# Kernel optimization log

Measured on AMD Instinct MI355X. Metric: run time of the kernel, lower is better.

Reference implementation:

```python
import jax, jax.numpy as jnp
import numpy as np

B, T, C = 2, 2048, 1024
H = 16
HD = C // H  # head_size = 64


def setup_inputs() -> dict:
    key = jax.random.key(0)
    k1, k2, k3 = jax.random.split(key, 3)
    x = jax.random.normal(k1, (B, T, C), dtype=jnp.float32)
    W_qkv = jax.random.normal(k2, (C, 3 * C), dtype=jnp.float32) * (1.0 / np.sqrt(C))
    b_qkv = jnp.zeros((3 * C,), dtype=jnp.float32)
    W_proj = jax.random.normal(k3, (C, C), dtype=jnp.float32) * (1.0 / np.sqrt(C))
    b_proj = jnp.zeros((C,), dtype=jnp.float32)
    return {"x": x, "W_qkv": W_qkv, "b_qkv": b_qkv, "W_proj": W_proj, "b_proj": b_proj}


def reference(x, W_qkv, b_qkv, W_proj, b_proj):
    Bc, Tc, Cc = x.shape
    qkv = x @ W_qkv + b_qkv                      # [B,T,3C]
    # Faithful to torch: view(B,T,H,3*HD) then chunk(3,-1) -> per-head interleaved split
    qkv = qkv.reshape(Bc, Tc, H, 3 * HD)
    q = qkv[..., 0 * HD:1 * HD]                  # [B,T,H,HD]
    k = qkv[..., 1 * HD:2 * HD]
    v = qkv[..., 2 * HD:3 * HD]
    # scores: [B,H,T,T]
    att = jnp.einsum('bqhd,bkhd->bhqk', q, k) / np.sqrt(HD)
    causal = jnp.tril(jnp.ones((Tc, Tc), dtype=bool))
    att = jnp.where(causal[None, None, :, :], att, -jnp.inf)
    att = jax.nn.softmax(att, axis=-1)
    out = jnp.einsum('bhqk,bkhd->bqhd', att, v).reshape(Bc, Tc, Cc)
    return out @ W_proj + b_proj
```

## Files before the change

kernel.cpp:

```cpp
#include <hip/hip_runtime.h>
#include <hip/hip_bf16.h>
#include <stdint.h>
#include <math.h>

#define T_SEQ 2048
#define NHEAD 16
#define CDIM 1024
#define QKV2_LD 2048

typedef __attribute__((ext_vector_type(8))) short short8;
typedef __attribute__((ext_vector_type(4))) short short4v;
typedef __attribute__((ext_vector_type(4))) float floatx4;

static __device__ __forceinline__ short bf16b(float f) {
    __hip_bfloat16 h = __float2bfloat16(f);
    return __builtin_bit_cast(short, h);
}

__global__ __launch_bounds__(256) void convert_f32_bf16(
    const float* __restrict__ in, __hip_bfloat16* __restrict__ out, int n)
{
    int i = (blockIdx.x * 256 + threadIdx.x) * 8;
    if (i >= n) return;
    float4 a = *(const float4*)(in + i);
    float4 b = *(const float4*)(in + i + 4);
    short8 o;
    o[0] = bf16b(a.x); o[1] = bf16b(a.y); o[2] = bf16b(a.z); o[3] = bf16b(a.w);
    o[4] = bf16b(b.x); o[5] = bf16b(b.y); o[6] = bf16b(b.z); o[7] = bf16b(b.w);
    *(short8*)(out + i) = o;
}

__global__ __launch_bounds__(256) void transpose_convert_kernel(
    const float* __restrict__ in, __hip_bfloat16* __restrict__ out,
    int R, int C)
{
    __shared__ short tile[64][65];
    const int r0 = blockIdx.y << 6;
    const int c0 = blockIdx.x << 6;
    const int tid = threadIdx.x;
    #pragma unroll
    for (int t = 0; t < 4; ++t) {
        int ch = t * 256 + tid;
        int rr = ch >> 4, cc = (ch & 15) << 2;
        float4 v = *(const float4*)(in + (size_t)(r0 + rr) * C + c0 + cc);
        tile[rr][cc + 0] = bf16b(v.x);
        tile[rr][cc + 1] = bf16b(v.y);
        tile[rr][cc + 2] = bf16b(v.z);
        tile[rr][cc + 3] = bf16b(v.w);
    }
    __syncthreads();
    #pragma unroll
    for (int t = 0; t < 2; ++t) {
        int ch = t * 256 + tid;
        int cc = ch >> 3, rr8 = (ch & 7) << 3;
        short8 v;
        #pragma unroll
        for (int j = 0; j < 8; ++j) v[j] = tile[rr8 + j][cc];
        *(short8*)(out + (size_t)(c0 + cc) * R + r0 + rr8) = v;
    }
}

template <int MI, int NI, int MINW, bool QKV, typename OutT>
__global__ __launch_bounds__(256, MINW) void gemm_bias_kernel(
    const __hip_bfloat16* __restrict__ A,
    const __hip_bfloat16* __restrict__ Bt,
    const float* __restrict__ bias,
    OutT* __restrict__ C,
    __hip_bfloat16* __restrict__ vT,
    int M, int N, int K)
{
    __shared__ short As[MI * 32 * 64];
    __shared__ short Bs[NI * 32 * 64];
    const int tid  = threadIdx.x;
    const int lane = tid & 63;
    const int w    = tid >> 6;
    const int quad = lane >> 4;
    const int c16  = lane & 15;
    const int m0 = blockIdx.x * (MI * 32);
    const int n0 = blockIdx.y * (NI * 32);
    const int wm = (w >> 1) * (MI * 16);
    const int wn = (w & 1) * (NI * 16);

    floatx4 acc[MI][NI] = {};

    for (int kt = 0; kt < K; kt += 64) {
        __syncthreads();
        #pragma unroll
        for (int r = 0; r < MI; ++r) {
            int ch = r * 256 + tid;
            int row = ch >> 3, k8 = (ch & 7) << 3;
            const __hip_bfloat16* ga = A + (size_t)(m0 + row) * K + kt + k8;
            __builtin_amdgcn_global_load_lds(
                (const __attribute__((address_space(1))) void*)ga,
                (__attribute__((address_space(3))) void*)&As[ch * 8], 16, 0, 0);
        }
        #pragma unroll
        for (int r = 0; r < NI; ++r) {
            int ch = r * 256 + tid;
            int row = ch >> 3, k8 = (ch & 7) << 3;
            const __hip_bfloat16* gb = Bt + (size_t)(n0 + row) * K + kt + k8;
            __builtin_amdgcn_global_load_lds(
                (const __attribute__((address_space(1))) void*)gb,
                (__attribute__((address_space(3))) void*)&Bs[ch * 8], 16, 0, 0);
        }
        __syncthreads();
        #pragma unroll
        for (int ko = 0; ko < 64; ko += 32) {
            short8 af[MI], bfr[NI];
            #pragma unroll
            for (int mi = 0; mi < MI; ++mi)
                af[mi] = *(const short8*)&As[(wm + mi * 16 + c16) * 64 + ko + quad * 8];
            #pragma unroll
            for (int ni = 0; ni < NI; ++ni)
                bfr[ni] = *(const short8*)&Bs[(wn + ni * 16 + c16) * 64 + ko + quad * 8];
            #pragma unroll
            for (int mi = 0; mi < MI; ++mi)
                #pragma unroll
                for (int ni = 0; ni < NI; ++ni)
                    acc[mi][ni] = __builtin_amdgcn_mfma_f32_16x16x32_bf16(
                        af[mi], bfr[ni], acc[mi][ni], 0, 0, 0);
        }
    }

    if constexpr (QKV) {
        const int colblk = (n0 + wn) >> 6;
        const int head = colblk / 3;
        const int kind = colblk % 3;
        const int b    = m0 >> 11;
        if (kind == 2) {
            const size_t vbase = ((size_t)(b * 16 + head)) * 64 * T_SEQ;
            #pragma unroll
            for (int mi = 0; mi < MI; ++mi) {
                int t0 = ((m0 + wm + mi * 16) & 2047) + quad * 4;
                #pragma unroll
                for (int ni = 0; ni < NI; ++ni) {
                    int hd = ni * 16 + c16;
                    float bv = bias[n0 + wn + hd];
                    short4v pk;
                    #pragma unroll
                    for (int r2 = 0; r2 < 4; ++r2)
                        pk[r2] = bf16b(acc[mi][ni][r2] + bv);
                    *(short4v*)(vT + vbase + (size_t)hd * T_SEQ + t0) = pk;
                }
            }
        } else {
            const int cbase = head * 128 + kind * 64;
            #pragma unroll
            for (int mi = 0; mi < MI; ++mi)
                #pragma unroll
                for (int ni = 0; ni < NI; ++ni) {
                    float bv = bias[n0 + wn + ni * 16 + c16];
                    int col = cbase + ni * 16 + c16;
                    #pragma unroll
                    for (int r2 = 0; r2 < 4; ++r2) {
                        int row = m0 + wm + mi * 16 + quad * 4 + r2;
                        C[(size_t)row * QKV2_LD + col] = __float2bfloat16(acc[mi][ni][r2] + bv);
                    }
                }
        }
    } else {
        #pragma unroll
        for (int mi = 0; mi < MI; ++mi)
            #pragma unroll
            for (int ni = 0; ni < NI; ++ni) {
                int col = n0 + wn + ni * 16 + c16;
                float bv = bias[col];
                #pragma unroll
                for (int r2 = 0; r2 < 4; ++r2) {
                    int row = m0 + wm + mi * 16 + quad * 4 + r2;
                    float v = acc[mi][ni][r2] + bv;
                    if constexpr (__is_same(OutT, float)) {
                        C[(size_t)row * N + col] = v;
                    } else {
                        C[(size_t)row * N + col] = __float2bfloat16(v);
                    }
                }
            }
    }
}

static __device__ __forceinline__ int pkey(int row) {
    return (row ^ ((row >> 2) << 1)) & 7;
}

__global__ __launch_bounds__(256, 2) void attn_kernel(
    const __hip_bfloat16* __restrict__ qkv,
    const __hip_bfloat16* __restrict__ vT,
    __hip_bfloat16* __restrict__ attn_out)
{
    __shared__ short Ks[2][128 * 64];
    __shared__ short Vs[2][64 * 128];
    __shared__ short Pl[4][16 * 128];

    const int hb = blockIdx.x;
    const int qt = blockIdx.y;
    const int h  = hb & 15;
    const int b  = hb >> 4;
    const int tid  = threadIdx.x;
    const int lane = tid & 63;
    const int w    = tid >> 6;
    const int quad = lane >> 4;
    const int c16  = lane & 15;

    const size_t rowbase = (size_t)b * T_SEQ;
    const size_t vbase   = (size_t)hb * 64 * T_SEQ;
    const int q0   = qt << 6;
    const int wrow = w << 4;
    const int hoff = h * 128;

    short8 qf[2];
    #pragma unroll
    for (int ko = 0; ko < 2; ++ko)
        qf[ko] = *(const short8*)(qkv +
            (rowbase + q0 + wrow + c16) * QKV2_LD + hoff + ko * 32 + quad * 8);

    floatx4 O[4] = {};
    floatx4 lpart = {0.f, 0.f, 0.f, 0.f};

    const float sc = 0.125f * 1.4426950408889634f;
    const int nkt = (qt >> 1) + 1;

    auto stage = [&](int kt, int bsel) {
        const int k0s = kt << 7;
        #pragma unroll
        for (int r = 0; r < 4; ++r) {
            int ch = r * 256 + tid;
            int krow = ch >> 3;
            int hc = (ch & 7) ^ (krow & 7);
            const __hip_bfloat16* g = qkv + (rowbase + k0s + krow) * QKV2_LD + hoff + 64 + hc * 8;
            __builtin_amdgcn_global_load_lds(
                (const __attribute__((address_space(1))) void*)g,
                (__attribute__((address_space(3))) void*)&Ks[bsel][ch * 8], 16, 0, 0);
        }
        #pragma unroll
        for (int r = 0; r < 4; ++r) {
            int ch = r * 256 + tid;
            int hd = ch >> 4;
            int kc = (ch & 15) ^ (hd & 7);
            const __hip_bfloat16* g = vT + vbase + (size_t)hd * T_SEQ + k0s + kc * 8;
            __builtin_amdgcn_global_load_lds(
                (const __attribute__((address_space(1))) void*)g,
                (__attribute__((address_space(3))) void*)&Vs[bsel][ch * 8], 16, 0, 0);
        }
    };

    stage(0, 0);
    int buf = 0;

    for (int kt = 0; kt < nkt; ++kt) {
        __syncthreads();
        if (kt + 1 < nkt) stage(kt + 1, buf ^ 1);

        floatx4 S[8] = {};
        #pragma unroll
        for (int ko = 0; ko < 2; ++ko) {
            short8 kf[8];
            #pragma unroll
            for (int ni = 0; ni < 8; ++ni)
                kf[ni] = *(const short8*)&Ks[buf][(ni * 16 + c16) * 64 +
                                                 (((4 * ko + quad) ^ (c16 & 7)) << 3)];
            #pragma unroll
            for (int ni = 0; ni < 8; ++ni)
                S[ni] = __builtin_amdgcn_mfma_f32_16x16x32_bf16(qf[ko], kf[ni], S[ni], 0, 0, 0);
        }

        const bool diag = (kt == nkt - 1);
        const int  moff = q0 - (kt << 7);
        #pragma unroll
        for (int ni = 0; ni < 8; ++ni)
            #pragma unroll
            for (int r = 0; r < 4; ++r) {
                bool msk = diag && (ni * 16 + c16 > wrow + quad * 4 + r + moff);
                float p = msk ? 0.f : exp2f(S[ni][r] * sc);
                S[ni][r] = p;
                lpart[r] += p;
            }

        #pragma unroll
        for (int ni = 0; ni < 8; ++ni)
            #pragma unroll
            for (int r = 0; r < 4; ++r) {
                int row = quad * 4 + r, col = ni * 16 + c16;
                Pl[w][row * 128 + (((col >> 3) ^ pkey(row)) << 3) + (col & 7)] = bf16b(S[ni][r]);
            }

        #pragma unroll
        for (int ko = 0; ko < 4; ++ko) {
            short8 pa = *(const short8*)&Pl[w][c16 * 128 + (((4 * ko + quad) ^ pkey(c16)) << 3)];
            short8 vb[4];
            #pragma unroll
            for (int ni = 0; ni < 4; ++ni)
                vb[ni] = *(const short8*)&Vs[buf][(ni * 16 + c16) * 128 +
                                                 (((4 * ko + quad) ^ (c16 & 7)) << 3)];
            #pragma unroll
            for (int ni = 0; ni < 4; ++ni)
                O[ni] = __builtin_amdgcn_mfma_f32_16x16x32_bf16(pa, vb[ni], O[ni], 0, 0, 0);
        }
        buf ^= 1;
    }

    #pragma unroll
    for (int r = 0; r < 4; ++r) {
        float l = lpart[r];
        l += __shfl_xor(l, 1);
        l += __shfl_xor(l, 2);
        l += __shfl_xor(l, 4);
        l += __shfl_xor(l, 8);
        float inv = 1.0f / l;
        size_t row = rowbase + q0 + wrow + quad * 4 + r;
        #pragma unroll
        for (int ni = 0; ni < 4; ++ni)
            attn_out[row * CDIM + h * 64 + ni * 16 + c16] =
                __float2bfloat16(O[ni][r] * inv);
    }
}

extern "C" void kernel_launch(void* const* d_in, const int* in_sizes, int n_in,
                              void* d_out, int out_size, void* d_ws, size_t ws_size,
                              hipStream_t stream) {
    const float* x     = (const float*)d_in[0];
    const float* Wqkv  = (const float*)d_in[1];
    const float* bqkv  = (const float*)d_in[2];
    const float* Wproj = (const float*)d_in[3];
    const float* bproj = (const float*)d_in[4];
    float* out = (float*)d_out;

    __hip_bfloat16* xb     = (__hip_bfloat16*)d_ws;
    __hip_bfloat16* WqkvT  = xb     + (size_t)4096 * 1024;
    __hip_bfloat16* WprojT = WqkvT  + (size_t)3072 * 1024;
    __hip_bfloat16* qkv2   = WprojT + (size_t)1024 * 1024;
    __hip_bfloat16* vT     = qkv2   + (size_t)4096 * 2048;
    __hip_bfloat16* attn   = vT     + (size_t)32 * 64 * 2048;

    convert_f32_bf16<<<4096 * 1024 / 2048, 256, 0, stream>>>(x, xb, 4096 * 1024);
    transpose_convert_kernel<<<dim3(3072 / 64, 1024 / 64), 256, 0, stream>>>(Wqkv, WqkvT, 1024, 3072);
    transpose_convert_kernel<<<dim3(1024 / 64, 1024 / 64), 256, 0, stream>>>(Wproj, WprojT, 1024, 1024);
    gemm_bias_kernel<4, 4, 2, true, __hip_bfloat16>
        <<<dim3(4096 / 128, 3072 / 128), 256, 0, stream>>>(
        xb, WqkvT, bqkv, qkv2, vT, 4096, 3072, 1024);
    attn_kernel<<<dim3(32, 32), 256, 0, stream>>>(qkv2, vT, attn);
    gemm_bias_kernel<4, 2, 2, false, float>
        <<<dim3(4096 / 128, 1024 / 64), 256, 0, stream>>>(
        attn, WprojT, bproj, out, nullptr, 4096, 1024, 1024);
}
```

Measured before the change: 199.8 us.

## Double-buffer GEMM LDS tiles and shrink attention key tiles to 64

The GEMM kernel gains double-buffered LDS staging, so the next K-slice is loaded while MFMAs run on the current one, and it now needs one barrier per iteration instead of two. The attention kernel moves from 128-wide to 64-wide key tiles with smaller LDS buffers, and raises its occupancy hint from 2 to 4 blocks. Its causal masking is split into a separate diagonal-tile branch, which drops the masked work past the diagonal at finer granularity. The projection GEMM's min-waves hint rises to 3; the trade-off is more loop iterations and barriers in attention and doubled LDS in the GEMMs.

```diff
diff --git a/kernel.cpp b/kernel.cpp
--- a/kernel.cpp
+++ b/kernel.cpp
@@ -69,8 +69,8 @@
     __hip_bfloat16* __restrict__ vT,
     int M, int N, int K)
 {
-    __shared__ short As[MI * 32 * 64];
-    __shared__ short Bs[NI * 32 * 64];
+    __shared__ short As[2][MI * 32 * 64];
+    __shared__ short Bs[2][NI * 32 * 64];
     const int tid  = threadIdx.x;
     const int lane = tid & 63;
     const int w    = tid >> 6;
@@ -83,36 +83,44 @@
 
     floatx4 acc[MI][NI] = {};
 
-    for (int kt = 0; kt < K; kt += 64) {
-        __syncthreads();
+    auto stage = [&](int kt, int bsel) {
+        const int ktoff = kt * 64;
         #pragma unroll
         for (int r = 0; r < MI; ++r) {
             int ch = r * 256 + tid;
             int row = ch >> 3, k8 = (ch & 7) << 3;
-            const __hip_bfloat16* ga = A + (size_t)(m0 + row) * K + kt + k8;
+            const __hip_bfloat16* ga = A + (size_t)(m0 + row) * K + ktoff + k8;
             __builtin_amdgcn_global_load_lds(
                 (const __attribute__((address_space(1))) void*)ga,
-                (__attribute__((address_space(3))) void*)&As[ch * 8], 16, 0, 0);
+                (__attribute__((address_space(3))) void*)&As[bsel][ch * 8], 16, 0, 0);
         }
         #pragma unroll
         for (int r = 0; r < NI; ++r) {
             int ch = r * 256 + tid;
             int row = ch >> 3, k8 = (ch & 7) << 3;
-            const __hip_bfloat16* gb = Bt + (size_t)(n0 + row) * K + kt + k8;
+            const __hip_bfloat16* gb = Bt + (size_t)(n0 + row) * K + ktoff + k8;
             __builtin_amdgcn_global_load_lds(
                 (const __attribute__((address_space(1))) void*)gb,
-                (__attribute__((address_space(3))) void*)&Bs[ch * 8], 16, 0, 0);
-        }
+                (__attribute__((address_space(3))) void*)&Bs[bsel][ch * 8], 16, 0, 0);
+        }
+    };
+
+    const int nk = K >> 6;
+    stage(0, 0);
+    int buf = 0;
+
+    for (int kt = 0; kt < nk; ++kt) {
         __syncthreads();
+        if (kt + 1 < nk) stage(kt + 1, buf ^ 1);
         #pragma unroll
         for (int ko = 0; ko < 64; ko += 32) {
             short8 af[MI], bfr[NI];
             #pragma unroll
             for (int mi = 0; mi < MI; ++mi)
-                af[mi] = *(const short8*)&As[(wm + mi * 16 + c16) * 64 + ko + quad * 8];
+                af[mi] = *(const short8*)&As[buf][(wm + mi * 16 + c16) * 64 + ko + quad * 8];
             #pragma unroll
             for (int ni = 0; ni < NI; ++ni)
-                bfr[ni] = *(const short8*)&Bs[(wn + ni * 16 + c16) * 64 + ko + quad * 8];
+                bfr[ni] = *(const short8*)&Bs[buf][(wn + ni * 16 + c16) * 64 + ko + quad * 8];
             #pragma unroll
             for (int mi = 0; mi < MI; ++mi)
                 #pragma unroll
@@ -120,6 +128,7 @@
                     acc[mi][ni] = __builtin_amdgcn_mfma_f32_16x16x32_bf16(
                         af[mi], bfr[ni], acc[mi][ni], 0, 0, 0);
         }
+        buf ^= 1;
     }
 
     if constexpr (QKV) {
@@ -179,18 +188,14 @@
     }
 }
 
-static __device__ __forceinline__ int pkey(int row) {
-    return (row ^ ((row >> 2) << 1)) & 7;
-}
-
-__global__ __launch_bounds__(256, 2) void attn_kernel(
+__global__ __launch_bounds__(256, 4) void attn_kernel(
     const __hip_bfloat16* __restrict__ qkv,
     const __hip_bfloat16* __restrict__ vT,
     __hip_bfloat16* __restrict__ attn_out)
 {
-    __shared__ short Ks[2][128 * 64];
-    __shared__ short Vs[2][64 * 128];
-    __shared__ short Pl[4][16 * 128];
+    __shared__ short Ks[2][64 * 64];
+    __shared__ short Vs[2][64 * 64];
+    __shared__ short Pl[4][16 * 64];
 
     const int hb = blockIdx.x;
     const int qt = blockIdx.y;
@@ -218,12 +223,12 @@
     floatx4 lpart = {0.f, 0.f, 0.f, 0.f};
 
     const float sc = 0.125f * 1.4426950408889634f;
-    const int nkt = (qt >> 1) + 1;
+    const int nkt = qt + 1;
 
     auto stage = [&](int kt, int bsel) {
-        const int k0s = kt << 7;
-        #pragma unroll
-        for (int r = 0; r < 4; ++r) {
+        const int k0s = kt << 6;
+        #pragma unroll
+        for (int r = 0; r < 2; ++r) {
             int ch = r * 256 + tid;
             int krow = ch >> 3;
             int hc = (ch & 7) ^ (krow & 7);
@@ -233,10 +238,10 @@
                 (__attribute__((address_space(3))) void*)&Ks[bsel][ch * 8], 16, 0, 0);
         }
         #pragma unroll
-        for (int r = 0; r < 4; ++r) {
+        for (int r = 0; r < 2; ++r) {
             int ch = r * 256 + tid;
-            int hd = ch >> 4;
-            int kc = (ch & 15) ^ (hd & 7);
+            int hd = ch >> 3;
+            int kc = (ch & 7) ^ (hd & 7);
             const __hip_bfloat16* g = vT + vbase + (size_t)hd * T_SEQ + k0s + kc * 8;
             __builtin_amdgcn_global_load_lds(
                 (const __attribute__((address_space(1))) void*)g,
@@ -251,46 +256,55 @@
         __syncthreads();
         if (kt + 1 < nkt) stage(kt + 1, buf ^ 1);
 
-        floatx4 S[8] = {};
+        floatx4 S[4] = {};
         #pragma unroll
         for (int ko = 0; ko < 2; ++ko) {
-            short8 kf[8];
-            #pragma unroll
-            for (int ni = 0; ni < 8; ++ni)
+            short8 kf[4];
+            #pragma unroll
+            for (int ni = 0; ni < 4; ++ni)
                 kf[ni] = *(const short8*)&Ks[buf][(ni * 16 + c16) * 64 +
                                                  (((4 * ko + quad) ^ (c16 & 7)) << 3)];
             #pragma unroll
-            for (int ni = 0; ni < 8; ++ni)
+            for (int ni = 0; ni < 4; ++ni)
                 S[ni] = __builtin_amdgcn_mfma_f32_16x16x32_bf16(qf[ko], kf[ni], S[ni], 0, 0, 0);
         }
 
-        const bool diag = (kt == nkt - 1);
-        const int  moff = q0 - (kt << 7);
-        #pragma unroll
-        for (int ni = 0; ni < 8; ++ni)
-            #pragma unroll
-            for (int r = 0; r < 4; ++r) {
-                bool msk = diag && (ni * 16 + c16 > wrow + quad * 4 + r + moff);
-                float p = msk ? 0.f : exp2f(S[ni][r] * sc);
-                S[ni][r] = p;
-                lpart[r] += p;
-            }
-
-        #pragma unroll
-        for (int ni = 0; ni < 8; ++ni)
+        if (kt == nkt - 1) {
+            #pragma unroll
+            for (int ni = 0; ni < 4; ++ni)
+                #pragma unroll
+                for (int r = 0; r < 4; ++r) {
+                    bool msk = (ni * 16 + c16 > wrow + quad * 4 + r);
+                    float p = msk ? 0.f : exp2f(S[ni][r] * sc);
+                    S[ni][r] = p;
+                    lpart[r] += p;
+                }
+        } else {
+            #pragma unroll
+            for (int ni = 0; ni < 4; ++ni)
+                #pragma unroll
+                for (int r = 0; r < 4; ++r) {
+                    float p = exp2f(S[ni][r] * sc);
+                    S[ni][r] = p;
+                    lpart[r] += p;
+                }
+        }
+
+        #pragma unroll
+        for (int ni = 0; ni < 4; ++ni)
             #pragma unroll
             for (int r = 0; r < 4; ++r) {
                 int row = quad * 4 + r, col = ni * 16 + c16;
-                Pl[w][row * 128 + (((col >> 3) ^ pkey(row)) << 3) + (col & 7)] = bf16b(S[ni][r]);
+                Pl[w][row * 64 + (((col >> 3) ^ (row & 7)) << 3) + (col & 7)] = bf16b(S[ni][r]);
             }
 
         #pragma unroll
-        for (int ko = 0; ko < 4; ++ko) {
-            short8 pa = *(const short8*)&Pl[w][c16 * 128 + (((4 * ko + quad) ^ pkey(c16)) << 3)];
+        for (int ko = 0; ko < 2; ++ko) {
+            short8 pa = *(const short8*)&Pl[w][c16 * 64 + (((4 * ko + quad) ^ (c16 & 7)) << 3)];
             short8 vb[4];
             #pragma unroll
             for (int ni = 0; ni < 4; ++ni)
-                vb[ni] = *(const short8*)&Vs[buf][(ni * 16 + c16) * 128 +
+                vb[ni] = *(const short8*)&Vs[buf][(ni * 16 + c16) * 64 +
                                                  (((4 * ko + quad) ^ (c16 & 7)) << 3)];
             #pragma unroll
             for (int ni = 0; ni < 4; ++ni)
@@ -339,7 +353,7 @@
         <<<dim3(4096 / 128, 3072 / 128), 256, 0, stream>>>(
         xb, WqkvT, bqkv, qkv2, vT, 4096, 3072, 1024);
     attn_kernel<<<dim3(32, 32), 256, 0, stream>>>(qkv2, vT, attn);
-    gemm_bias_kernel<4, 2, 2, false, float>
+    gemm_bias_kernel<4, 2, 3, false, float>
         <<<dim3(4096 / 128, 1024 / 64), 256, 0, stream>>>(
         attn, WprojT, bproj, out, nullptr, 4096, 1024, 1024);
 }
```

New measurement: 208.6 us. 1.04x slower.
